# Optimization experiments

Measured on AMD Instinct MI355X. Metric: run time of the kernel, lower is better.

The kernel has to match this reference:

```python
import jax, jax.numpy as jnp
import numpy as np

K_MAX = 8
R_C = 5.0

def chebyshev_basis(r, r_c, k_max):
    # Smooth cutoff fc(r) and Chebyshev recurrence T_k(x), x in [-1, 1]
    fc = jnp.where(r < r_c, 0.5 * jnp.cos(jnp.pi * r / r_c) + 0.5, jnp.zeros_like(r))
    x = 2.0 * (r / r_c - 1.0) ** 2 - 1.0
    fn = [jnp.ones_like(x)]
    if k_max > 1:
        fn.append(x)
        for _ in range(2, k_max):
            fn.append(2.0 * x * fn[-1] - fn[-2])
    fn = jnp.stack(fn, axis=-1)              # [E, k_max]
    return (fn + 1.0) * (0.5 * fc)[..., None]


def setup_inputs() -> dict:
    key = jax.random.key(0)
    k1, k2, k3, k4 = jax.random.split(key, 4)
    E = 4_000_000
    n_types, n_desc = 8, 8
    r_ij = jax.random.uniform(k1, (E,), dtype=jnp.float32)
    type_i = jax.random.randint(k2, (E,), 0, n_types, dtype=jnp.int64)
    type_j = jax.random.randint(k3, (E,), 0, n_types, dtype=jnp.int64)
    c_table = jax.random.normal(k4, (n_types, n_types, n_desc, K_MAX), dtype=jnp.float32)
    return {"r_ij": r_ij, "type_i": type_i, "type_j": type_j, "c_table": c_table}


def reference(r_ij, type_i, type_j, c_table):
    f = chebyshev_basis(r_ij, R_C, K_MAX)        # [E, k]
    c = c_table[type_i, type_j]                  # [E, n_desc, k] gather per type-pair
    g = jnp.einsum('edk,ek->ed', c, f)           # sum over k -> [E, n_desc]
    return g
```

## Files before the change

kernel.cpp:

```cpp
#include <hip/hip_runtime.h>


#define KMAX 8
#define NDESC 8

__global__ __launch_bounds__(256, 4) void radial_kernel(
    const float* __restrict__ r_ij,
    const int*   __restrict__ type_i,
    const int*   __restrict__ type_j,
    const float* __restrict__ c_table,
    float*       __restrict__ out,
    int E)
{
    __shared__ float lds[64 * 64];
    const int tid = threadIdx.x;
    for (int i = tid; i < 4096; i += 256) {
        int p = i >> 6, j = i & 63;
        lds[(j << 6) | p] = c_table[i];
    }
    __syncthreads();

    const int stride = gridDim.x * blockDim.x;
    for (int e = blockIdx.x * blockDim.x + tid; e < E; e += stride) {
        float r = r_ij[e];
        int   p = (type_i[e] << 3) | type_j[e];

        float fc = (r < 5.0f) ? (0.5f * __cosf(0.62831853071795864769f * r) + 0.5f)
                              : 0.0f;
        float u = r * 0.2f - 1.0f;
        float x = 2.0f * u * u - 1.0f;
        float h = 0.5f * fc;

        float f[KMAX];
        f[0] = fc;
        f[1] = (x + 1.0f) * h;
        float t_prev = 1.0f, t_cur = x;
        #pragma unroll
        for (int k = 2; k < KMAX; ++k) {
            float t = 2.0f * x * t_cur - t_prev;
            t_prev = t_cur; t_cur = t;
            f[k] = (t + 1.0f) * h;
        }

        float acc[NDESC];
        #pragma unroll
        for (int d = 0; d < NDESC; ++d) acc[d] = 0.0f;

        const float* colbase = lds + p;
        #pragma unroll
        for (int d = 0; d < NDESC; ++d) {
            #pragma unroll
            for (int k = 0; k < KMAX; ++k) {
                acc[d] = fmaf(colbase[((d << 3) | k) << 6], f[k], acc[d]);
            }
        }

        float4* o = reinterpret_cast<float4*>(out + (size_t)e * 8);
        o[0] = make_float4(acc[0], acc[1], acc[2], acc[3]);
        o[1] = make_float4(acc[4], acc[5], acc[6], acc[7]);
    }
}

extern "C" void kernel_launch(void* const* d_in, const int* in_sizes, int n_in,
                              void* d_out, int out_size, void* d_ws, size_t ws_size,
                              hipStream_t stream) {
    const float* r_ij   = (const float*)d_in[0];
    const int*   type_i = (const int*)d_in[1];
    const int*   type_j = (const int*)d_in[2];
    const float* c_tab  = (const float*)d_in[3];
    float* out = (float*)d_out;
    int E = in_sizes[0];

    dim3 block(256);
    dim3 grid(2048);
    radial_kernel<<<grid, block, 0, stream>>>(r_ij, type_i, type_j, c_tab, out, E);
}
```

Baseline: 190.5 us.

## Store coefficient table as fp16 rows in LDS with vector reads and nontemporal stores

Converts the per-type-pair coefficient table to half precision and stores it row-major in LDS with a padded stride, so each descriptor's 8 coefficients come in one 16-byte LDS read instead of 8 scalar strided reads. Output writes become nontemporal vector stores to avoid polluting cache with streaming output. The change reduces LDS instruction count and footprint but lowers coefficient precision to fp16, which may exceed tolerance.

```diff
diff --git a/kernel.cpp b/kernel.cpp
--- a/kernel.cpp
+++ b/kernel.cpp
@@ -1,8 +1,31 @@
 #include <hip/hip_runtime.h>
+#include <hip/hip_fp16.h>
 
 
 #define KMAX 8
 #define NDESC 8
+#define HSTRIDE 72
+
+typedef float f32x4 __attribute__((ext_vector_type(4)));
+
+struct alignas(16) Half8 { __half2 h[4]; };
+
+__device__ __forceinline__ void edge_basis(float r, float* __restrict__ f) {
+    float fc = (r < 5.0f) ? (0.5f * __cosf(0.62831853071795864769f * r) + 0.5f)
+                          : 0.0f;
+    float u = r * 0.2f - 1.0f;
+    float x = 2.0f * u * u - 1.0f;
+    float h = 0.5f * fc;
+    f[0] = fc;
+    f[1] = (x + 1.0f) * h;
+    float t_prev = 1.0f, t_cur = x;
+    #pragma unroll
+    for (int k = 2; k < KMAX; ++k) {
+        float t = 2.0f * x * t_cur - t_prev;
+        t_prev = t_cur; t_cur = t;
+        f[k] = (t + 1.0f) * h;
+    }
+}
 
 __global__ __launch_bounds__(256, 4) void radial_kernel(
     const float* __restrict__ r_ij,
@@ -12,11 +35,18 @@
     float*       __restrict__ out,
     int E)
 {
-    __shared__ float lds[64 * 64];
+    __shared__ __half lds_h[64 * HSTRIDE];
     const int tid = threadIdx.x;
-    for (int i = tid; i < 4096; i += 256) {
-        int p = i >> 6, j = i & 63;
-        lds[(j << 6) | p] = c_table[i];
+    for (int cidx = tid; cidx < 512; cidx += 256) {
+        const float4 v0 = reinterpret_cast<const float4*>(c_table)[cidx * 2];
+        const float4 v1 = reinterpret_cast<const float4*>(c_table)[cidx * 2 + 1];
+        Half8 hv;
+        hv.h[0] = __floats2half2_rn(v0.x, v0.y);
+        hv.h[1] = __floats2half2_rn(v0.z, v0.w);
+        hv.h[2] = __floats2half2_rn(v1.x, v1.y);
+        hv.h[3] = __floats2half2_rn(v1.z, v1.w);
+        int p = cidx >> 3, d = cidx & 7;
+        *reinterpret_cast<Half8*>(&lds_h[p * HSTRIDE + d * 8]) = hv;
     }
     __syncthreads();
 
@@ -25,39 +55,35 @@
         float r = r_ij[e];
         int   p = (type_i[e] << 3) | type_j[e];
 
-        float fc = (r < 5.0f) ? (0.5f * __cosf(0.62831853071795864769f * r) + 0.5f)
-                              : 0.0f;
-        float u = r * 0.2f - 1.0f;
-        float x = 2.0f * u * u - 1.0f;
-        float h = 0.5f * fc;
+        float f[KMAX];
+        edge_basis(r, f);
 
-        float f[KMAX];
-        f[0] = fc;
-        f[1] = (x + 1.0f) * h;
-        float t_prev = 1.0f, t_cur = x;
-        #pragma unroll
-        for (int k = 2; k < KMAX; ++k) {
-            float t = 2.0f * x * t_cur - t_prev;
-            t_prev = t_cur; t_cur = t;
-            f[k] = (t + 1.0f) * h;
-        }
+        const __half* rowbase = &lds_h[p * HSTRIDE];
 
         float acc[NDESC];
         #pragma unroll
-        for (int d = 0; d < NDESC; ++d) acc[d] = 0.0f;
-
-        const float* colbase = lds + p;
-        #pragma unroll
         for (int d = 0; d < NDESC; ++d) {
-            #pragma unroll
-            for (int k = 0; k < KMAX; ++k) {
-                acc[d] = fmaf(colbase[((d << 3) | k) << 6], f[k], acc[d]);
-            }
+            Half8 ch = *reinterpret_cast<const Half8*>(rowbase + d * 8);
+            float2 c01 = __half22float2(ch.h[0]);
+            float2 c23 = __half22float2(ch.h[1]);
+            float2 c45 = __half22float2(ch.h[2]);
+            float2 c67 = __half22float2(ch.h[3]);
+            float a = c01.x * f[0];
+            a = fmaf(c01.y, f[1], a);
+            a = fmaf(c23.x, f[2], a);
+            a = fmaf(c23.y, f[3], a);
+            a = fmaf(c45.x, f[4], a);
+            a = fmaf(c45.y, f[5], a);
+            a = fmaf(c67.x, f[6], a);
+            a = fmaf(c67.y, f[7], a);
+            acc[d] = a;
         }
 
-        float4* o = reinterpret_cast<float4*>(out + (size_t)e * 8);
-        o[0] = make_float4(acc[0], acc[1], acc[2], acc[3]);
-        o[1] = make_float4(acc[4], acc[5], acc[6], acc[7]);
+        f32x4* o = reinterpret_cast<f32x4*>(out + (size_t)e * 8);
+        f32x4 v0 = { acc[0], acc[1], acc[2], acc[3] };
+        f32x4 v1 = { acc[4], acc[5], acc[6], acc[7] };
+        __builtin_nontemporal_store(v0, o);
+        __builtin_nontemporal_store(v1, o + 1);
     }
 }
 
```

Result: faster. 183.2 us (-3.9%).
